# Optimization experiments

Measured on AMD Instinct MI355X. Metric: run time of the kernel, lower is better.

Reference implementation:

```python
import jax, jax.numpy as jnp
import numpy as np

N_NODES = 30000
N_EDGES = 480000
T_STEPS = 8
F_IN = 8
HID = 32
K = 5
PERIODS = 8


def setup_inputs() -> dict:
    key = jax.random.key(0)
    ks = jax.random.split(key, 9)
    timesteps = jax.random.normal(ks[0], (T_STEPS, N_NODES, F_IN), jnp.float32)
    src = jax.random.randint(ks[1], (N_EDGES,), 0, N_NODES)
    dst = jax.random.randint(ks[2], (N_EDGES,), 0, N_NODES)
    edge_index = jnp.stack([src, dst])
    # ChebConv weights for gates [i, f, c, o]; glorot-ish scale
    Wx = jax.random.normal(ks[3], (4, K, F_IN, HID), jnp.float32) * (1.0 / np.sqrt(F_IN))
    Wh = jax.random.normal(ks[4], (4, K, HID, HID), jnp.float32) * (1.0 / np.sqrt(HID))
    w_c = jax.random.normal(ks[5], (3, HID), jnp.float32) * 0.1  # peepholes for i, f, o
    b_gates = jax.random.normal(ks[6], (4, HID), jnp.float32) * 0.1  # b_i, b_f, b_c, b_o
    W_lin = jax.random.normal(ks[7], (PERIODS, HID), jnp.float32) * (1.0 / np.sqrt(HID))
    b_lin = jax.random.normal(ks[8], (PERIODS,), jnp.float32) * 0.1
    return {"timesteps": timesteps, "edge_index": edge_index, "Wx": Wx, "Wh": Wh,
            "w_c": w_c, "b_gates": b_gates, "W_lin": W_lin, "b_lin": b_lin}


def reference(timesteps, edge_index, Wx, Wh, w_c, b_gates, W_lin, b_lin):
    N = timesteps.shape[1]
    src, dst = edge_index[0], edge_index[1]
    # get_laplacian('sym') removes self loops, deg over edge rows; with lambda_max=2,
    # L_hat = 2L/lmax - I = -D^{-1/2} A D^{-1/2} (diag: 1 from L plus added -1 self loop = 0)
    w = jnp.where(src != dst, 1.0, 0.0).astype(timesteps.dtype)
    deg = jax.ops.segment_sum(w, src, num_segments=N)
    dis = jnp.where(deg > 0, 1.0 / jnp.sqrt(jnp.where(deg > 0, deg, 1.0)), 0.0)
    norm = dis[src] * w * dis[dst]  # [E]

    def lap(x):  # x: [N, C] -> L_hat @ x
        return -jax.ops.segment_sum(norm[:, None] * x[src], dst, num_segments=N)

    def cheb(x, W):  # Chebyshev recurrence; W: [K, in, out]
        Tx0 = x
        out = Tx0 @ W[0]
        Tx1 = lap(Tx0)
        out = out + Tx1 @ W[1]
        for k in range(2, W.shape[0]):
            Tx2 = 2.0 * lap(Tx1) - Tx0
            out = out + Tx2 @ W[k]
            Tx0, Tx1 = Tx1, Tx2
        return out

    def step(carry, x):
        H, C = carry
        I = jax.nn.sigmoid(cheb(x, Wx[0]) + cheb(H, Wh[0]) + w_c[0] * C + b_gates[0])
        Fg = jax.nn.sigmoid(cheb(x, Wx[1]) + cheb(H, Wh[1]) + w_c[1] * C + b_gates[1])
        Tg = jnp.tanh(cheb(x, Wx[2]) + cheb(H, Wh[2]) + b_gates[2])
        Cn = Fg * C + I * Tg
        O = jax.nn.sigmoid(cheb(x, Wx[3]) + cheb(H, Wh[3]) + w_c[2] * Cn + b_gates[3])
        Hn = O * jnp.tanh(Cn)
        return (Hn, Cn), None

    hid = Wh.shape[-1]
    H0 = jnp.zeros((N, hid), timesteps.dtype)
    (H, C), _ = jax.lax.scan(step, (H0, H0), timesteps)
    return jax.nn.relu(H) @ W_lin.T + b_lin
```

## Files before the change

### kernel.cpp

```cpp
#include <hip/hip_runtime.h>
#include <hip/hip_fp16.h>
#include <math.h>

#define T_STEPS 8
#define F_IN    8
#define HID     32
#define KCH     5
#define PERIODS 8

typedef __attribute__((ext_vector_type(8))) _Float16 half8_t;
typedef __attribute__((ext_vector_type(4))) float    f32x4_t;

__device__ __forceinline__ float sigmoidf_(float x) { return 1.f / (1.f + __expf(-x)); }
__device__ __forceinline__ float tanhf_(float x) {
    float e = __expf(2.f * x);
    return 1.f - 2.f / (e + 1.f);
}


__global__ void k_count(const int* __restrict__ src, const int* __restrict__ dst,
                        int* __restrict__ degi, int* __restrict__ cnt, int E) {
    int e = blockIdx.x * blockDim.x + threadIdx.x;
    if (e >= E) return;
    int s = src[e], d = dst[e];
    if (s != d) {
        atomicAdd(&degi[s], 1);
        atomicAdd(&cnt[d], 1);
    }
}

__global__ void k_hist2(const int* __restrict__ cnt, int* __restrict__ hist,
                        int N, int NT) {
    __shared__ int h[256];
    int tid = threadIdx.x, blk = blockIdx.x;
    h[tid] = 0;
    __syncthreads();
    int n = blk * 256 + tid;
    if (n < N) atomicAdd(&h[min(cnt[n], 255)], 1);
    __syncthreads();
    hist[tid * NT + blk] = h[tid];
}

__global__ void __launch_bounds__(1024) k_scan(const int* __restrict__ in,
                                               int* __restrict__ outp, int n) {
    __shared__ int wsum[16];
    int tid = threadIdx.x;
    int base = tid * 32;
    int v[32];
    int s = 0;
    #pragma unroll
    for (int i = 0; i < 32; ++i) {
        int idx = base + i;
        int t = (idx < n) ? in[idx] : 0;
        v[i] = t; s += t;
    }
    int lane = tid & 63, wave = tid >> 6;
    int incl = s;
    #pragma unroll
    for (int off = 1; off < 64; off <<= 1) {
        int t = __shfl_up(incl, off, 64);
        if (lane >= off) incl += t;
    }
    if (lane == 63) wsum[wave] = incl;
    __syncthreads();
    if (tid < 64) {
        int w = (tid < 16) ? wsum[tid] : 0;
        int iw = w;
        #pragma unroll
        for (int off = 1; off < 16; off <<= 1) {
            int t = __shfl_up(iw, off, 64);
            if (tid >= off) iw += t;
        }
        if (tid < 16) wsum[tid] = iw - w;
    }
    __syncthreads();
    int excl = wsum[wave] + (incl - s);
    #pragma unroll
    for (int i = 0; i < 32; ++i) {
        int idx = base + i;
        if (idx < n) outp[idx] = excl;
        excl += v[i];
    }
    if (tid == 1023) outp[n] = wsum[15] + incl;
}

__global__ void k_permscat2(const int* __restrict__ cnt, const int* __restrict__ degi,
                            const int* __restrict__ histbase,
                            int* __restrict__ perm, int* __restrict__ iperm,
                            int* __restrict__ cntp, float* __restrict__ dis,
                            int N, int NT) {
    __shared__ int key[256];
    int tid = threadIdx.x, blk = blockIdx.x;
    int n = blk * 256 + tid;
    int k = (n < N) ? min(cnt[n], 255) : -1;
    key[tid] = k;
    __syncthreads();
    if (n < N) {
        int r = 0;
        for (int j = 0; j < tid; ++j) r += (key[j] == k);
        int pos = histbase[k * NT + blk] + r;
        perm[pos] = n;
        iperm[n] = pos;
        cntp[pos] = cnt[n];
        int dg = degi[n];
        dis[n] = (dg > 0) ? rsqrtf((float)dg) : 0.f;
    }
}

__global__ void k_scatxt(const int* __restrict__ src, const int* __restrict__ dst,
                         const float* __restrict__ dis, const int* __restrict__ rowptr,
                         const int* __restrict__ iperm, int* __restrict__ fill,
                         unsigned int* __restrict__ cv, const float* __restrict__ xall,
                         __half* __restrict__ xb,
                         const float* __restrict__ Wh, __half* __restrict__ Bpack,
                         const float* __restrict__ Wx, __half* __restrict__ Bxpack,
                         int N, int E) {
    int gsz = (int)(gridDim.x * blockDim.x);
    int gtid = blockIdx.x * blockDim.x + threadIdx.x;
    for (int e = gtid; e < E; e += gsz) {
        int s = src[e], d = dst[e];
        if (s != d) {
            float nv = -dis[s] * dis[d];
            unsigned short h16 = __half_as_ushort(__float2half(nv));
            int dp = iperm[d];
            int p = atomicAdd(&fill[dp], 1);
            cv[rowptr[dp] + p] = (unsigned int)(unsigned short)iperm[s]
                               | ((unsigned int)h16 << 16);
        }
    }
    for (int i = gtid; i < N * T_STEPS; i += gsz) {
        int n = i >> 3, t = i & 7;
        float4 a = *(const float4*)(xall + ((size_t)t * N + n) * 8);
        float4 b = *(const float4*)(xall + ((size_t)t * N + n) * 8 + 4);
        __half2 h[4];
        h[0] = __float22half2_rn(make_float2(a.x, a.y));
        h[1] = __float22half2_rn(make_float2(a.z, a.w));
        h[2] = __float22half2_rn(make_float2(b.x, b.y));
        h[3] = __float22half2_rn(make_float2(b.z, b.w));
        *(float4*)(xb + (size_t)iperm[n] * 64 + t * 8) = *(float4*)h;
    }
    for (int i = gtid; i < KCH * 8 * 64 * 8; i += gsz) {
        int j = i & 7, lane = (i >> 3) & 63, nt = (i >> 9) & 7, k = i >> 12;
        int col = lane & 15, quad = lane >> 4;
        int kk = quad * 8 + j;
        int o = nt * 16 + col, g = o >> 5, h = o & 31;
        Bpack[i] = __float2half(Wh[(((g * KCH + k) * 32) + kk) * 32 + h]);
    }
    for (int i = gtid; i < 2 * 8 * 64 * 8; i += gsz) {
        int j = i & 7, lane = (i >> 3) & 63, nt = (i >> 9) & 7, c = i >> 12;
        int col = lane & 15, quad = lane >> 4;
        int kk = c * 32 + quad * 8 + j;
        int kcheb = kk >> 3, ch = kk & 7;
        int o = nt * 16 + col, g = o >> 5, h = o & 31;
        float v = (kcheb < KCH) ? Wx[(((g * KCH + kcheb) * 8) + ch) * 32 + h] : 0.f;
        Bxpack[i] = __float2half(v);
    }
}

template <int C, int ES>
__device__ __forceinline__ void lap_body(__half* __restrict__ outp,
                                         const __half* __restrict__ xin,
                                         const __half* __restrict__ xprev,
                                         float alpha, float beta,
                                         const int* __restrict__ rowptr,
                                         const unsigned int* __restrict__ cv,
                                         int N, int g) {
    constexpr int Q = C / 8;
    constexpr int W = Q * ES;
    int idx = g * 256 + (int)threadIdx.x;
    int node = idx / W;
    int r = idx % W;
    int q = r % Q, s = r / Q;
    if (node >= N) node = N - 1;
    int beg = rowptr[node], end = rowptr[node + 1];
    float a0 = 0.f, a1 = 0.f, a2 = 0.f, a3 = 0.f, a4 = 0.f, a5 = 0.f, a6 = 0.f, a7 = 0.f;
    #pragma unroll 8
    for (int j = beg + s; j < end; j += ES) {
        unsigned int pv = cv[j];
        int pcol = (int)(pv & 0xffffu);
        float nv = __half2float(__ushort_as_half((unsigned short)(pv >> 16)));
        float4 raw = *(const float4*)(xin + (size_t)pcol * C + q * 8);
        const __half2* h = (const __half2*)&raw;
        float2 f0 = __half22float2(h[0]);
        float2 f1 = __half22float2(h[1]);
        float2 f2 = __half22float2(h[2]);
        float2 f3 = __half22float2(h[3]);
        a0 += nv * f0.x; a1 += nv * f0.y; a2 += nv * f1.x; a3 += nv * f1.y;
        a4 += nv * f2.x; a5 += nv * f2.y; a6 += nv * f3.x; a7 += nv * f3.y;
    }
    #pragma unroll
    for (int m = Q; m < W; m <<= 1) {
        a0 += __shfl_xor(a0, m, 64); a1 += __shfl_xor(a1, m, 64);
        a2 += __shfl_xor(a2, m, 64); a3 += __shfl_xor(a3, m, 64);
        a4 += __shfl_xor(a4, m, 64); a5 += __shfl_xor(a5, m, 64);
        a6 += __shfl_xor(a6, m, 64); a7 += __shfl_xor(a7, m, 64);
    }
    if (s == 0) {
        size_t off = (size_t)node * C + q * 8;
        float r0 = alpha * a0, r1 = alpha * a1, r2 = alpha * a2, r3 = alpha * a3;
        float r4 = alpha * a4, r5 = alpha * a5, r6 = alpha * a6, r7 = alpha * a7;
        if (beta != 0.f) {
            float4 raw = *(const float4*)(xprev + off);
            const __half2* h = (const __half2*)&raw;
            float2 f0 = __half22float2(h[0]);
            float2 f1 = __half22float2(h[1]);
            float2 f2 = __half22float2(h[2]);
            float2 f3 = __half22float2(h[3]);
            r0 += beta * f0.x; r1 += beta * f0.y; r2 += beta * f1.x; r3 += beta * f1.y;
            r4 += beta * f2.x; r5 += beta * f2.y; r6 += beta * f3.x; r7 += beta * f3.y;
        }
        __half2 o[4];
        o[0] = __float22half2_rn(make_float2(r0, r1));
        o[1] = __float22half2_rn(make_float2(r2, r3));
        o[2] = __float22half2_rn(make_float2(r4, r5));
        o[3] = __float22half2_rn(make_float2(r6, r7));
        *(float4*)(outp + off) = *(float4*)o;
    }
}

template <int C, int ES>
__global__ void __launch_bounds__(256) k_lap_h(__half* __restrict__ outp,
                                               const __half* __restrict__ xin,
                                               const __half* __restrict__ xprev,
                                               float alpha, float beta,
                                               const int* __restrict__ rowptr,
                                               const unsigned int* __restrict__ cv,
                                               int N) {
    lap_body<C, ES>(outp, xin, xprev, alpha, beta, rowptr, cv, N, blockIdx.x);
}

__device__ __forceinline__ void step_body(
    const __half* __restrict__ xb, const __half* __restrict__ TXB,
    __half* __restrict__ THall, float* __restrict__ Cst,
    const __half* __restrict__ Bpack, const __half* __restrict__ Bxpack,
    const float* __restrict__ w_c, const float* __restrict__ bg,
    const float* __restrict__ W_lin, const float* __restrict__ b_lin,
    const int* __restrict__ perm, float* __restrict__ out,
    const int* __restrict__ rowptr, const unsigned int* __restrict__ cv,
    int t, int doOut, int N, int g,
    __half* __restrict__ T4s, float* __restrict__ FOs, float* __restrict__ Hs) {
    int tid = (int)threadIdx.x;
    int base = g * 16;
    int lane = tid & 63, wv = tid >> 6;
    int col = lane & 15, quad = lane >> 4;

    {
        const __half* T3 = THall + (size_t)3 * N * HID;
        const __half* T2 = THall + (size_t)2 * N * HID;
        int nl = tid >> 4;
        int r = tid & 15;
        int q = r & 3, s = r >> 2;
        int node = base + nl; if (node >= N) node = N - 1;
        int beg = rowptr[node], end = rowptr[node + 1];
        float a0 = 0.f, a1 = 0.f, a2 = 0.f, a3 = 0.f, a4 = 0.f, a5 = 0.f, a6 = 0.f, a7 = 0.f;
        #pragma unroll 8
        for (int j = beg + s; j < end; j += 4) {
            unsigned int pv = cv[j];
            int pcol = (int)(pv & 0xffffu);
            float nv = __half2float(__ushort_as_half((unsigned short)(pv >> 16)));
            float4 raw = *(const float4*)(T3 + (size_t)pcol * HID + q * 8);
            const __half2* h = (const __half2*)&raw;
            float2 f0 = __half22float2(h[0]);
            float2 f1 = __half22float2(h[1]);
            float2 f2 = __half22float2(h[2]);
            float2 f3 = __half22float2(h[3]);
            a0 += nv * f0.x; a1 += nv * f0.y; a2 += nv * f1.x; a3 += nv * f1.y;
            a4 += nv * f2.x; a5 += nv * f2.y; a6 += nv * f3.x; a7 += nv * f3.y;
        }
        #pragma unroll
        for (int m = 4; m < 16; m <<= 1) {
            a0 += __shfl_xor(a0, m, 64); a1 += __shfl_xor(a1, m, 64);
            a2 += __shfl_xor(a2, m, 64); a3 += __shfl_xor(a3, m, 64);
            a4 += __shfl_xor(a4, m, 64); a5 += __shfl_xor(a5, m, 64);
            a6 += __shfl_xor(a6, m, 64); a7 += __shfl_xor(a7, m, 64);
        }
        if (s == 0) {
            float4 raw = *(const float4*)(T2 + (size_t)node * HID + q * 8);
            const __half2* h = (const __half2*)&raw;
            float2 f0 = __half22float2(h[0]);
            float2 f1 = __half22float2(h[1]);
            float2 f2 = __half22float2(h[2]);
            float2 f3 = __half22float2(h[3]);
            __half2 o[4];
            o[0] = __float22half2_rn(make_float2(2.f * a0 - f0.x, 2.f * a1 - f0.y));
            o[1] = __float22half2_rn(make_float2(2.f * a2 - f1.x, 2.f * a3 - f1.y));
            o[2] = __float22half2_rn(make_float2(2.f * a4 - f2.x, 2.f * a5 - f2.y));
            o[3] = __float22half2_rn(make_float2(2.f * a6 - f3.x, 2.f * a7 - f3.y));
            *(float4*)(T4s + nl * 32 + q * 8) = *(float4*)o;
        }
    }
    __syncthreads();

    int node_a = base + col; if (node_a >= N) node_a = N - 1;
    f32x4_t acc[2];
    #pragma unroll
    for (int i = 0; i < 2; ++i) {
        float b = bg[(wv + 4 * i) * 16 + col];
        acc[i][0] = b; acc[i][1] = b; acc[i][2] = b; acc[i][3] = b;
    }
    const half8_t* Bx = (const half8_t*)Bxpack;
    const half8_t* Bp = (const half8_t*)Bpack;
    {
        const __half* sp0 = (quad == 0)
            ? (xb + (size_t)node_a * 64 + t * 8)
            : (TXB + ((size_t)(quad - 1) * N + node_a) * 64 + t * 8);
        half8_t ax0 = *(const half8_t*)sp0;
        half8_t ax1 = {};
        if (quad == 0)
            ax1 = *(const half8_t*)(TXB + ((size_t)3 * N + node_a) * 64 + t * 8);
        #pragma unroll
        for (int i = 0; i < 2; ++i) {
            int nt = wv + 4 * i;
            acc[i] = __builtin_amdgcn_mfma_f32_16x16x32_f16(ax0, Bx[nt * 64 + lane], acc[i], 0, 0, 0);
            acc[i] = __builtin_amdgcn_mfma_f32_16x16x32_f16(ax1, Bx[(8 + nt) * 64 + lane], acc[i], 0, 0, 0);
        }
    }
    #pragma unroll
    for (int k = 0; k < 4; ++k) {
        half8_t a = *(const half8_t*)(THall + ((size_t)k * N + node_a) * 32 + quad * 8);
        #pragma unroll
        for (int i = 0; i < 2; ++i) {
            int nt = wv + 4 * i;
            acc[i] = __builtin_amdgcn_mfma_f32_16x16x32_f16(a, Bp[(k * 8 + nt) * 64 + lane], acc[i], 0, 0, 0);
        }
    }
    {
        half8_t a = *(const half8_t*)(T4s + col * 32 + quad * 8);
        #pragma unroll
        for (int i = 0; i < 2; ++i) {
            int nt = wv + 4 * i;
            acc[i] = __builtin_amdgcn_mfma_f32_16x16x32_f16(a, Bp[(4 * 8 + nt) * 64 + lane], acc[i], 0, 0, 0);
        }
    }

    if (wv >= 2) {
        int h = (wv - 2) * 16 + col;
        #pragma unroll
        for (int reg = 0; reg < 4; ++reg) {
            int nl = quad * 4 + reg;
            FOs[nl * 64 + h]      = acc[0][reg];
            FOs[nl * 64 + 32 + h] = acc[1][reg];
        }
    }
    __syncthreads();

    if (wv < 2) {
        int h = wv * 16 + col;
        #pragma unroll
        for (int reg = 0; reg < 4; ++reg) {
            int nl = quad * 4 + reg;
            int node = base + nl;
            if (node < N) {
                size_t idx = (size_t)node * 32 + h;
                float Co = Cst[idx];
                float I  = sigmoidf_(acc[0][reg] + w_c[h] * Co);
                float F  = sigmoidf_(FOs[nl * 64 + h] + w_c[32 + h] * Co);
                float Tg = tanhf_(acc[1][reg]);
                float Cn = F * Co + I * Tg;
                float O  = sigmoidf_(FOs[nl * 64 + 32 + h] + w_c[64 + h] * Cn);
                float Hn = O * tanhf_(Cn);
                Cst[idx] = Cn;
                THall[idx] = __float2half(Hn);
                if (doOut) Hs[nl * 33 + h] = fmaxf(Hn, 0.f);
            } else if (doOut) {
                Hs[nl * 33 + h] = 0.f;
            }
        }
    }

    if (doOut) {
        __syncthreads();
        if (tid < 128) {
            int nl = tid >> 3, pp = tid & 7;
            int node = base + nl;
            if (node < N) {
                float a0 = b_lin[pp];
                const float* hp = Hs + nl * 33;
                #pragma unroll
                for (int h = 0; h < HID; ++h)
                    a0 += hp[h] * W_lin[pp * HID + h];
                out[(size_t)perm[node] * PERIODS + pp] = a0;
            }
        }
    }
}

__global__ void __launch_bounds__(256) k_lapstep(
    const __half* __restrict__ xb, const __half* __restrict__ TXB,
    __half* __restrict__ THall, float* __restrict__ Cst,
    const __half* __restrict__ Bpack, const __half* __restrict__ Bxpack,
    const float* __restrict__ w_c, const float* __restrict__ bg,
    const float* __restrict__ W_lin, const float* __restrict__ b_lin,
    const int* __restrict__ perm, float* __restrict__ out,
    const int* __restrict__ rowptr, const unsigned int* __restrict__ cv,
    int t, int doOut, int N) {
    __shared__ __half T4s[16 * 32];
    __shared__ float FOs[16 * 64];
    __shared__ float Hs[16 * 33];
    step_body(xb, TXB, THall, Cst, Bpack, Bxpack, w_c, bg, W_lin, b_lin,
              perm, out, rowptr, cv, t, doOut, N, blockIdx.x, T4s, FOs, Hs);
}

__device__ __forceinline__ void step0_body(
    const __half* __restrict__ xb, const __half* __restrict__ TXB,
    __half* __restrict__ TXB3, __half* __restrict__ THall, float* __restrict__ Cst,
    const __half* __restrict__ Bxpack,
    const float* __restrict__ w_c, const float* __restrict__ bg,
    const int* __restrict__ rowptr, const unsigned int* __restrict__ cv,
    int N, int g, __half* __restrict__ X3s, float* __restrict__ FOs) {
    int tid = (int)threadIdx.x;
    int base = g * 16;
    int lane = tid & 63, wv = tid >> 6;
    int col = lane & 15, quad = lane >> 4;

    {
        const __half* T2 = TXB + (size_t)2 * N * 64;
        const __half* T1 = TXB + (size_t)1 * N * 64;
        int nl = tid >> 4;
        int r = tid & 15;
        int q = r & 7, s = r >> 3;
        int node = base + nl; if (node >= N) node = N - 1;
        int beg = rowptr[node], end = rowptr[node + 1];
        float a0 = 0.f, a1 = 0.f, a2 = 0.f, a3 = 0.f, a4 = 0.f, a5 = 0.f, a6 = 0.f, a7 = 0.f;
        #pragma unroll 8
        for (int j = beg + s; j < end; j += 2) {
            unsigned int pv = cv[j];
            int pcol = (int)(pv & 0xffffu);
            float nv = __half2float(__ushort_as_half((unsigned short)(pv >> 16)));
            float4 raw = *(const float4*)(T2 + (size_t)pcol * 64 + q * 8);
            const __half2* h = (const __half2*)&raw;
            float2 f0 = __half22float2(h[0]);
            float2 f1 = __half22float2(h[1]);
            float2 f2 = __half22float2(h[2]);
            float2 f3 = __half22float2(h[3]);
            a0 += nv * f0.x; a1 += nv * f0.y; a2 += nv * f1.x; a3 += nv * f1.y;
            a4 += nv * f2.x; a5 += nv * f2.y; a6 += nv * f3.x; a7 += nv * f3.y;
        }
        a0 += __shfl_xor(a0, 8, 64); a1 += __shfl_xor(a1, 8, 64);
        a2 += __shfl_xor(a2, 8, 64); a3 += __shfl_xor(a3, 8, 64);
        a4 += __shfl_xor(a4, 8, 64); a5 += __shfl_xor(a5, 8, 64);
        a6 += __shfl_xor(a6, 8, 64); a7 += __shfl_xor(a7, 8, 64);
        if (s == 0) {
            size_t off = (size_t)node * 64 + q * 8;
            float4 raw = *(const float4*)(T1 + off);
            const __half2* h = (const __half2*)&raw;
            float2 f0 = __half22float2(h[0]);
            float2 f1 = __half22float2(h[1]);
            float2 f2 = __half22float2(h[2]);
            float2 f3 = __half22float2(h[3]);
            __half2 o[4];
            o[0] = __float22half2_rn(make_float2(2.f * a0 - f0.x, 2.f * a1 - f0.y));
            o[1] = __float22half2_rn(make_float2(2.f * a2 - f1.x, 2.f * a3 - f1.y));
            o[2] = __float22half2_rn(make_float2(2.f * a4 - f2.x, 2.f * a5 - f2.y));
            o[3] = __float22half2_rn(make_float2(2.f * a6 - f3.x, 2.f * a7 - f3.y));
            *(float4*)(TXB3 + off) = *(float4*)o;
            *(float4*)(X3s + nl * 64 + q * 8) = *(float4*)o;
        }
    }
    __syncthreads();

    int node_a = base + col; if (node_a >= N) node_a = N - 1;
    f32x4_t acc[2];
    #pragma unroll
    for (int i = 0; i < 2; ++i) {
        float b = bg[(wv + 4 * i) * 16 + col];
        acc[i][0] = b; acc[i][1] = b; acc[i][2] = b; acc[i][3] = b;
    }
    const half8_t* Bx = (const half8_t*)Bxpack;
    {
        const __half* sp0 = (quad == 0)
            ? (xb + (size_t)node_a * 64)
            : (TXB + ((size_t)(quad - 1) * N + node_a) * 64);
        half8_t ax0 = *(const half8_t*)sp0;
        half8_t ax1 = {};
        if (quad == 0)
            ax1 = *(const half8_t*)(X3s + col * 64);
        #pragma unroll
        for (int i = 0; i < 2; ++i) {
            int nt = wv + 4 * i;
            acc[i] = __builtin_amdgcn_mfma_f32_16x16x32_f16(ax0, Bx[nt * 64 + lane], acc[i], 0, 0, 0);
            acc[i] = __builtin_amdgcn_mfma_f32_16x16x32_f16(ax1, Bx[(8 + nt) * 64 + lane], acc[i], 0, 0, 0);
        }
    }
    __syncthreads();

    if (wv >= 2) {
        int h = (wv - 2) * 16 + col;
        #pragma unroll
        for (int reg = 0; reg < 4; ++reg) {
            int nl = quad * 4 + reg;
            FOs[nl * 64 + h]      = acc[0][reg];
            FOs[nl * 64 + 32 + h] = acc[1][reg];
        }
    }
    __syncthreads();

    if (wv < 2) {
        int h = wv * 16 + col;
        #pragma unroll
        for (int reg = 0; reg < 4; ++reg) {
            int nl = quad * 4 + reg;
            int node = base + nl;
            if (node < N) {
                size_t idx = (size_t)node * 32 + h;
                float I  = sigmoidf_(acc[0][reg]);
                float Tg = tanhf_(acc[1][reg]);
                float Cn = I * Tg;
                float O  = sigmoidf_(FOs[nl * 64 + 32 + h] + w_c[64 + h] * Cn);
                Cst[idx] = Cn;
                THall[idx] = __float2half(O * tanhf_(Cn));
            }
        }
    }
}

__global__ void __launch_bounds__(256) k_lapstep0(
    const __half* __restrict__ xb, const __half* __restrict__ TXB,
    __half* __restrict__ TXB3, __half* __restrict__ THall, float* __restrict__ Cst,
    const __half* __restrict__ Bxpack,
    const float* __restrict__ w_c, const float* __restrict__ bg,
    const int* __restrict__ rowptr, const unsigned int* __restrict__ cv, int N) {
    __shared__ float FOs[16 * 64];
    step0_body(xb, TXB, TXB3, THall, Cst, Bxpack, w_c, bg, rowptr, cv, N,
               blockIdx.x, (__half*)FOs, FOs);
}


extern "C" void kernel_launch(void* const* d_in, const int* in_sizes, int n_in,
                              void* d_out, int out_size, void* d_ws, size_t ws_size,
                              hipStream_t stream) {
    const float* xall  = (const float*)d_in[0];
    const int*   ei    = (const int*)d_in[1];
    const float* Wx    = (const float*)d_in[2];
    const float* Wh    = (const float*)d_in[3];
    const float* w_c   = (const float*)d_in[4];
    const float* bg    = (const float*)d_in[5];
    const float* W_lin = (const float*)d_in[6];
    const float* b_lin = (const float*)d_in[7];
    float* out = (float*)d_out;

    const int E = in_sizes[1] / 2;
    const int N = in_sizes[0] / (T_STEPS * F_IN);
    const int NT = (N + 255) / 256;
    const int* src = ei;
    const int* dst = ei + E;

    char* p = (char*)d_ws;
    auto carve = [&](size_t bytes) -> void* {
        void* r = (void*)p;
        p += (bytes + 255) & ~(size_t)255;
        return r;
    };
    char* zero_begin = p;
    int*    degi  = (int*)   carve((size_t)N * 4);
    int*    cnt   = (int*)   carve((size_t)N * 4);
    int*    fill  = (int*)   carve((size_t)N * 4);
    float*  Cst   = (float*) carve((size_t)N * HID * 4);
    size_t zero_bytes = (size_t)(p - zero_begin);
    __half* THall = (__half*)carve((size_t)4 * N * HID * 2);
    int*    hist     = (int*)   carve((size_t)256 * NT * 4);
    int*    histbase = (int*)   carve(((size_t)256 * NT + 1) * 4);
    float*  dis      = (float*) carve((size_t)N * 4);
    int*    perm     = (int*)   carve((size_t)N * 4);
    int*    iperm    = (int*)   carve((size_t)N * 4);
    int*    cntp     = (int*)   carve((size_t)N * 4);
    int*    rowptr   = (int*)   carve((size_t)(N + 1) * 4);
    unsigned int* cv = (unsigned int*)carve((size_t)E * 4);
    __half* xb       = (__half*)carve((size_t)N * 64 * 2);
    __half* TXB      = (__half*)carve((size_t)4 * N * 64 * 2);
    __half* Bpack    = (__half*)carve((size_t)KCH * 8 * 64 * 8 * 2);
    __half* Bxpack   = (__half*)carve((size_t)2 * 8 * 64 * 8 * 2);

    hipMemsetAsync(zero_begin, 0, zero_bytes, stream);

    const int TB = 256;
    const int gE = (E + TB - 1) / TB;
    k_count<<<gE, TB, 0, stream>>>(src, dst, degi, cnt, E);
    k_hist2<<<NT, TB, 0, stream>>>(cnt, hist, N, NT);
    k_scan<<<1, 1024, 0, stream>>>(hist, histbase, 256 * NT);
    k_permscat2<<<NT, TB, 0, stream>>>(cnt, degi, histbase, perm, iperm, cntp, dis, N, NT);
    k_scan<<<1, 1024, 0, stream>>>(cntp, rowptr, N);
    k_scatxt<<<gE, TB, 0, stream>>>(src, dst, dis, rowptr, iperm, fill, cv, xall, xb,
                                    Wh, Bpack, Wx, Bxpack, N, E);

    __half* TXB0 = TXB;
    __half* TXB1 = TXB + (size_t)N * 64;
    __half* TXB2 = TXB + (size_t)2 * N * 64;
    __half* TXB3 = TXB + (size_t)3 * N * 64;
    const int lapx_grid = (N * 8 + TB - 1) / TB;
    k_lap_h<64, 1><<<lapx_grid, TB, 0, stream>>>(TXB0, xb,   nullptr, 1.f,  0.f, rowptr, cv, N);
    k_lap_h<64, 1><<<lapx_grid, TB, 0, stream>>>(TXB1, TXB0, xb,      2.f, -1.f, rowptr, cv, N);
    k_lap_h<64, 1><<<lapx_grid, TB, 0, stream>>>(TXB2, TXB1, TXB0,    2.f, -1.f, rowptr, cv, N);

    const int lapstep_grid = (N + 15) / 16;
    const int laph_grid = (N * 8 + TB - 1) / TB;
    __half* TH0 = THall;
    __half* TH1 = THall + (size_t)N * HID;
    __half* TH2 = THall + (size_t)2 * N * HID;
    __half* TH3 = THall + (size_t)3 * N * HID;

    k_lapstep0<<<lapstep_grid, TB, 0, stream>>>(xb, TXB, TXB3, THall, Cst, Bxpack,
                                                w_c, bg, rowptr, cv, N);
    for (int t = 1; t < T_STEPS; ++t) {
        k_lap_h<HID, 2><<<laph_grid, TB, 0, stream>>>(TH1, TH0, nullptr, 1.f,  0.f, rowptr, cv, N);
        k_lap_h<HID, 2><<<laph_grid, TB, 0, stream>>>(TH2, TH1, TH0,     2.f, -1.f, rowptr, cv, N);
        k_lap_h<HID, 2><<<laph_grid, TB, 0, stream>>>(TH3, TH2, TH1,     2.f, -1.f, rowptr, cv, N);
        k_lapstep<<<lapstep_grid, TB, 0, stream>>>(xb, TXB, THall, Cst, Bpack, Bxpack,
                                                   w_c, bg, W_lin, b_lin, perm, out,
                                                   rowptr, cv, t,
                                                   (t == T_STEPS - 1) ? 1 : 0, N);
    }
}
```

Baseline: 588.1 us.

## Drop degree-sorted node permutation and shrink step kernels to 128 threads

Removes the histogram, bucket sort and permutation kernels that reordered nodes by in-degree. CSR is now built directly in original node order with fewer preprocessing launches, and the dis computation moves into the scan kernel. The fused step kernels drop from 256 to 128 threads, with each wave holding all four gate accumulators, so the shared-memory exchange of the F/O gates and one barrier go away. The cost is losing degree-sorted load balance and locality in the gather kernels, and each step block now has less parallelism per node.

```diff
diff --git a/kernel.cpp b/kernel.cpp
--- a/kernel.cpp
+++ b/kernel.cpp
@@ -18,114 +18,19 @@
 }
 
 
-__global__ void k_count(const int* __restrict__ src, const int* __restrict__ dst,
-                        int* __restrict__ degi, int* __restrict__ cnt, int E) {
-    int e = blockIdx.x * blockDim.x + threadIdx.x;
-    if (e >= E) return;
-    int s = src[e], d = dst[e];
-    if (s != d) {
-        atomicAdd(&degi[s], 1);
-        atomicAdd(&cnt[d], 1);
-    }
-}
-
-__global__ void k_hist2(const int* __restrict__ cnt, int* __restrict__ hist,
-                        int N, int NT) {
-    __shared__ int h[256];
-    int tid = threadIdx.x, blk = blockIdx.x;
-    h[tid] = 0;
-    __syncthreads();
-    int n = blk * 256 + tid;
-    if (n < N) atomicAdd(&h[min(cnt[n], 255)], 1);
-    __syncthreads();
-    hist[tid * NT + blk] = h[tid];
-}
-
-__global__ void __launch_bounds__(1024) k_scan(const int* __restrict__ in,
-                                               int* __restrict__ outp, int n) {
-    __shared__ int wsum[16];
-    int tid = threadIdx.x;
-    int base = tid * 32;
-    int v[32];
-    int s = 0;
-    #pragma unroll
-    for (int i = 0; i < 32; ++i) {
-        int idx = base + i;
-        int t = (idx < n) ? in[idx] : 0;
-        v[i] = t; s += t;
-    }
-    int lane = tid & 63, wave = tid >> 6;
-    int incl = s;
-    #pragma unroll
-    for (int off = 1; off < 64; off <<= 1) {
-        int t = __shfl_up(incl, off, 64);
-        if (lane >= off) incl += t;
-    }
-    if (lane == 63) wsum[wave] = incl;
-    __syncthreads();
-    if (tid < 64) {
-        int w = (tid < 16) ? wsum[tid] : 0;
-        int iw = w;
-        #pragma unroll
-        for (int off = 1; off < 16; off <<= 1) {
-            int t = __shfl_up(iw, off, 64);
-            if (tid >= off) iw += t;
-        }
-        if (tid < 16) wsum[tid] = iw - w;
-    }
-    __syncthreads();
-    int excl = wsum[wave] + (incl - s);
-    #pragma unroll
-    for (int i = 0; i < 32; ++i) {
-        int idx = base + i;
-        if (idx < n) outp[idx] = excl;
-        excl += v[i];
-    }
-    if (tid == 1023) outp[n] = wsum[15] + incl;
-}
-
-__global__ void k_permscat2(const int* __restrict__ cnt, const int* __restrict__ degi,
-                            const int* __restrict__ histbase,
-                            int* __restrict__ perm, int* __restrict__ iperm,
-                            int* __restrict__ cntp, float* __restrict__ dis,
-                            int N, int NT) {
-    __shared__ int key[256];
-    int tid = threadIdx.x, blk = blockIdx.x;
-    int n = blk * 256 + tid;
-    int k = (n < N) ? min(cnt[n], 255) : -1;
-    key[tid] = k;
-    __syncthreads();
-    if (n < N) {
-        int r = 0;
-        for (int j = 0; j < tid; ++j) r += (key[j] == k);
-        int pos = histbase[k * NT + blk] + r;
-        perm[pos] = n;
-        iperm[n] = pos;
-        cntp[pos] = cnt[n];
-        int dg = degi[n];
-        dis[n] = (dg > 0) ? rsqrtf((float)dg) : 0.f;
-    }
-}
-
-__global__ void k_scatxt(const int* __restrict__ src, const int* __restrict__ dst,
-                         const float* __restrict__ dis, const int* __restrict__ rowptr,
-                         const int* __restrict__ iperm, int* __restrict__ fill,
-                         unsigned int* __restrict__ cv, const float* __restrict__ xall,
-                         __half* __restrict__ xb,
-                         const float* __restrict__ Wh, __half* __restrict__ Bpack,
-                         const float* __restrict__ Wx, __half* __restrict__ Bxpack,
-                         int N, int E) {
+__global__ void k_prep(const int* __restrict__ src, const int* __restrict__ dst,
+                       int* __restrict__ degi, int* __restrict__ cnt,
+                       const float* __restrict__ xall, __half* __restrict__ xb,
+                       const float* __restrict__ Wh, __half* __restrict__ Bpack,
+                       const float* __restrict__ Wx, __half* __restrict__ Bxpack,
+                       int N, int E) {
     int gsz = (int)(gridDim.x * blockDim.x);
     int gtid = blockIdx.x * blockDim.x + threadIdx.x;
     for (int e = gtid; e < E; e += gsz) {
         int s = src[e], d = dst[e];
         if (s != d) {
-            float nv = -dis[s] * dis[d];
-            unsigned short h16 = __half_as_ushort(__float2half(nv));
-            int dp = iperm[d];
-            int p = atomicAdd(&fill[dp], 1);
-            cv[rowptr[dp] + p] = (unsigned int)(unsigned short)iperm[s]
-                               | ((unsigned int)h16 << 16);
+            atomicAdd(&degi[s], 1);
+            atomicAdd(&cnt[d], 1);
         }
     }
     for (int i = gtid; i < N * T_STEPS; i += gsz) {
@@ -137,7 +42,7 @@
         h[1] = __float22half2_rn(make_float2(a.z, a.w));
         h[2] = __float22half2_rn(make_float2(b.x, b.y));
         h[3] = __float22half2_rn(make_float2(b.z, b.w));
-        *(float4*)(xb + (size_t)iperm[n] * 64 + t * 8) = *(float4*)h;
+        *(float4*)(xb + (size_t)n * 64 + t * 8) = *(float4*)h;
     }
     for (int i = gtid; i < KCH * 8 * 64 * 8; i += gsz) {
         int j = i & 7, lane = (i >> 3) & 63, nt = (i >> 9) & 7, k = i >> 12;
@@ -154,6 +59,72 @@
         int o = nt * 16 + col, g = o >> 5, h = o & 31;
         float v = (kcheb < KCH) ? Wx[(((g * KCH + kcheb) * 8) + ch) * 32 + h] : 0.f;
         Bxpack[i] = __float2half(v);
+    }
+}
+
+__global__ void __launch_bounds__(1024) k_scan2(const int* __restrict__ in,
+                                                int* __restrict__ outp, int n,
+                                                const int* __restrict__ degi,
+                                                float* __restrict__ dis) {
+    __shared__ int wsum[16];
+    int tid = threadIdx.x;
+    for (int i = tid; i < n; i += 1024) {
+        int dg = degi[i];
+        dis[i] = (dg > 0) ? rsqrtf((float)dg) : 0.f;
+    }
+    int base = tid * 32;
+    int v[32];
+    int s = 0;
+    #pragma unroll
+    for (int i = 0; i < 32; ++i) {
+        int idx = base + i;
+        int t = (idx < n) ? in[idx] : 0;
+        v[i] = t; s += t;
+    }
+    int lane = tid & 63, wave = tid >> 6;
+    int incl = s;
+    #pragma unroll
+    for (int off = 1; off < 64; off <<= 1) {
+        int t = __shfl_up(incl, off, 64);
+        if (lane >= off) incl += t;
+    }
+    if (lane == 63) wsum[wave] = incl;
+    __syncthreads();
+    if (tid < 64) {
+        int w = (tid < 16) ? wsum[tid] : 0;
+        int iw = w;
+        #pragma unroll
+        for (int off = 1; off < 16; off <<= 1) {
+            int t = __shfl_up(iw, off, 64);
+            if (tid >= off) iw += t;
+        }
+        if (tid < 16) wsum[tid] = iw - w;
+    }
+    __syncthreads();
+    int excl = wsum[wave] + (incl - s);
+    #pragma unroll
+    for (int i = 0; i < 32; ++i) {
+        int idx = base + i;
+        if (idx < n) outp[idx] = excl;
+        excl += v[i];
+    }
+    if (tid == 1023) outp[n] = wsum[15] + incl;
+}
+
+__global__ void k_scat(const int* __restrict__ src, const int* __restrict__ dst,
+                       const float* __restrict__ dis, const int* __restrict__ rowptr,
+                       int* __restrict__ fill, unsigned int* __restrict__ cv, int E) {
+    int gsz = (int)(gridDim.x * blockDim.x);
+    int gtid = blockIdx.x * blockDim.x + threadIdx.x;
+    for (int e = gtid; e < E; e += gsz) {
+        int s = src[e], d = dst[e];
+        if (s != d) {
+            float nv = -dis[s] * dis[d];
+            unsigned short h16 = __half_as_ushort(__float2half(nv));
+            int p = atomicAdd(&fill[d], 1);
+            cv[rowptr[d] + p] = (unsigned int)(unsigned short)s
+                              | ((unsigned int)h16 << 16);
+        }
     }
 }
 
@@ -235,26 +206,26 @@
     const __half* __restrict__ Bpack, const __half* __restrict__ Bxpack,
     const float* __restrict__ w_c, const float* __restrict__ bg,
     const float* __restrict__ W_lin, const float* __restrict__ b_lin,
-    const int* __restrict__ perm, float* __restrict__ out,
+    float* __restrict__ out,
     const int* __restrict__ rowptr, const unsigned int* __restrict__ cv,
     int t, int doOut, int N, int g,
-    __half* __restrict__ T4s, float* __restrict__ FOs, float* __restrict__ Hs) {
+    __half* __restrict__ T4s, float* __restrict__ Hs) {
     int tid = (int)threadIdx.x;
     int base = g * 16;
-    int lane = tid & 63, wv = tid >> 6;
+    int lane = tid & 63, w = tid >> 6;
     int col = lane & 15, quad = lane >> 4;
 
     {
         const __half* T3 = THall + (size_t)3 * N * HID;
         const __half* T2 = THall + (size_t)2 * N * HID;
-        int nl = tid >> 4;
-        int r = tid & 15;
+        int nl = tid >> 3;
+        int r = tid & 7;
         int q = r & 3, s = r >> 2;
         int node = base + nl; if (node >= N) node = N - 1;
         int beg = rowptr[node], end = rowptr[node + 1];
         float a0 = 0.f, a1 = 0.f, a2 = 0.f, a3 = 0.f, a4 = 0.f, a5 = 0.f, a6 = 0.f, a7 = 0.f;
         #pragma unroll 8
-        for (int j = beg + s; j < end; j += 4) {
+        for (int j = beg + s; j < end; j += 2) {
             unsigned int pv = cv[j];
             int pcol = (int)(pv & 0xffffu);
             float nv = __half2float(__ushort_as_half((unsigned short)(pv >> 16)));
@@ -267,13 +238,10 @@
             a0 += nv * f0.x; a1 += nv * f0.y; a2 += nv * f1.x; a3 += nv * f1.y;
             a4 += nv * f2.x; a5 += nv * f2.y; a6 += nv * f3.x; a7 += nv * f3.y;
         }
-        #pragma unroll
-        for (int m = 4; m < 16; m <<= 1) {
-            a0 += __shfl_xor(a0, m, 64); a1 += __shfl_xor(a1, m, 64);
-            a2 += __shfl_xor(a2, m, 64); a3 += __shfl_xor(a3, m, 64);
-            a4 += __shfl_xor(a4, m, 64); a5 += __shfl_xor(a5, m, 64);
-            a6 += __shfl_xor(a6, m, 64); a7 += __shfl_xor(a7, m, 64);
-        }
+        a0 += __shfl_xor(a0, 4, 64); a1 += __shfl_xor(a1, 4, 64);
+        a2 += __shfl_xor(a2, 4, 64); a3 += __shfl_xor(a3, 4, 64);
+        a4 += __shfl_xor(a4, 4, 64); a5 += __shfl_xor(a5, 4, 64);
+        a6 += __shfl_xor(a6, 4, 64); a7 += __shfl_xor(a7, 4, 64);
         if (s == 0) {
             float4 raw = *(const float4*)(T2 + (size_t)node * HID + q * 8);
             const __half2* h = (const __half2*)&raw;
@@ -292,11 +260,11 @@
     __syncthreads();
 
     int node_a = base + col; if (node_a >= N) node_a = N - 1;
-    f32x4_t acc[2];
-    #pragma unroll
-    for (int i = 0; i < 2; ++i) {
-        float b = bg[(wv + 4 * i) * 16 + col];
-        acc[i][0] = b; acc[i][1] = b; acc[i][2] = b; acc[i][3] = b;
+    f32x4_t acc[4];
+    #pragma unroll
+    for (int gi = 0; gi < 4; ++gi) {
+        float b = bg[(2 * gi + w) * 16 + col];
+        acc[gi][0] = b; acc[gi][1] = b; acc[gi][2] = b; acc[gi][3] = b;
     }
     const half8_t* Bx = (const half8_t*)Bxpack;
     const half8_t* Bp = (const half8_t*)Bpack;
@@ -309,43 +277,32 @@
         if (quad == 0)
             ax1 = *(const half8_t*)(TXB + ((size_t)3 * N + node_a) * 64 + t * 8);
         #pragma unroll
-        for (int i = 0; i < 2; ++i) {
-            int nt = wv + 4 * i;
-            acc[i] = __builtin_amdgcn_mfma_f32_16x16x32_f16(ax0, Bx[nt * 64 + lane], acc[i], 0, 0, 0);
-            acc[i] = __builtin_amdgcn_mfma_f32_16x16x32_f16(ax1, Bx[(8 + nt) * 64 + lane], acc[i], 0, 0, 0);
+        for (int gi = 0; gi < 4; ++gi) {
+            int nt = 2 * gi + w;
+            acc[gi] = __builtin_amdgcn_mfma_f32_16x16x32_f16(ax0, Bx[nt * 64 + lane], acc[gi], 0, 0, 0);
+            acc[gi] = __builtin_amdgcn_mfma_f32_16x16x32_f16(ax1, Bx[(8 + nt) * 64 + lane], acc[gi], 0, 0, 0);
         }
     }
     #pragma unroll
     for (int k = 0; k < 4; ++k) {
         half8_t a = *(const half8_t*)(THall + ((size_t)k * N + node_a) * 32 + quad * 8);
         #pragma unroll
-        for (int i = 0; i < 2; ++i) {
-            int nt = wv + 4 * i;
-            acc[i] = __builtin_amdgcn_mfma_f32_16x16x32_f16(a, Bp[(k * 8 + nt) * 64 + lane], acc[i], 0, 0, 0);
+        for (int gi = 0; gi < 4; ++gi) {
+            int nt = 2 * gi + w;
+            acc[gi] = __builtin_amdgcn_mfma_f32_16x16x32_f16(a, Bp[(k * 8 + nt) * 64 + lane], acc[gi], 0, 0, 0);
         }
     }
     {
         half8_t a = *(const half8_t*)(T4s + col * 32 + quad * 8);
         #pragma unroll
-        for (int i = 0; i < 2; ++i) {
-            int nt = wv + 4 * i;
-            acc[i] = __builtin_amdgcn_mfma_f32_16x16x32_f16(a, Bp[(4 * 8 + nt) * 64 + lane], acc[i], 0, 0, 0);
-        }
-    }
-
-    if (wv >= 2) {
-        int h = (wv - 2) * 16 + col;
-        #pragma unroll
-        for (int reg = 0; reg < 4; ++reg) {
-            int nl = quad * 4 + reg;
-            FOs[nl * 64 + h]      = acc[0][reg];
-            FOs[nl * 64 + 32 + h] = acc[1][reg];
-        }
-    }
-    __syncthreads();
-
-    if (wv < 2) {
-        int h = wv * 16 + col;
+        for (int gi = 0; gi < 4; ++gi) {
+            int nt = 2 * gi + w;
+            acc[gi] = __builtin_amdgcn_mfma_f32_16x16x32_f16(a, Bp[(4 * 8 + nt) * 64 + lane], acc[gi], 0, 0, 0);
+        }
+    }
+
+    {
+        int h = w * 16 + col;
         #pragma unroll
         for (int reg = 0; reg < 4; ++reg) {
             int nl = quad * 4 + reg;
@@ -354,10 +311,10 @@
                 size_t idx = (size_t)node * 32 + h;
                 float Co = Cst[idx];
                 float I  = sigmoidf_(acc[0][reg] + w_c[h] * Co);
-                float F  = sigmoidf_(FOs[nl * 64 + h] + w_c[32 + h] * Co);
-                float Tg = tanhf_(acc[1][reg]);
+                float F  = sigmoidf_(acc[1][reg] + w_c[32 + h] * Co);
+                float Tg = tanhf_(acc[2][reg]);
                 float Cn = F * Co + I * Tg;
-                float O  = sigmoidf_(FOs[nl * 64 + 32 + h] + w_c[64 + h] * Cn);
+                float O  = sigmoidf_(acc[3][reg] + w_c[64 + h] * Cn);
                 float Hn = O * tanhf_(Cn);
                 Cst[idx] = Cn;
                 THall[idx] = __float2half(Hn);
@@ -370,35 +327,32 @@
 
     if (doOut) {
         __syncthreads();
-        if (tid < 128) {
-            int nl = tid >> 3, pp = tid & 7;
-            int node = base + nl;
-            if (node < N) {
-                float a0 = b_lin[pp];
-                const float* hp = Hs + nl * 33;
-                #pragma unroll
-                for (int h = 0; h < HID; ++h)
-                    a0 += hp[h] * W_lin[pp * HID + h];
-                out[(size_t)perm[node] * PERIODS + pp] = a0;
-            }
-        }
-    }
-}
-
-__global__ void __launch_bounds__(256) k_lapstep(
+        int nl = tid >> 3, pp = tid & 7;
+        int node = base + nl;
+        if (node < N) {
+            float a0 = b_lin[pp];
+            const float* hp = Hs + nl * 33;
+            #pragma unroll
+            for (int h = 0; h < HID; ++h)
+                a0 += hp[h] * W_lin[pp * HID + h];
+            out[(size_t)node * PERIODS + pp] = a0;
+        }
+    }
+}
+
+__global__ void __launch_bounds__(128) k_lapstep(
     const __half* __restrict__ xb, const __half* __restrict__ TXB,
     __half* __restrict__ THall, float* __restrict__ Cst,
     const __half* __restrict__ Bpack, const __half* __restrict__ Bxpack,
     const float* __restrict__ w_c, const float* __restrict__ bg,
     const float* __restrict__ W_lin, const float* __restrict__ b_lin,
-    const int* __restrict__ perm, float* __restrict__ out,
+    float* __restrict__ out,
     const int* __restrict__ rowptr, const unsigned int* __restrict__ cv,
     int t, int doOut, int N) {
     __shared__ __half T4s[16 * 32];
-    __shared__ float FOs[16 * 64];
     __shared__ float Hs[16 * 33];
     step_body(xb, TXB, THall, Cst, Bpack, Bxpack, w_c, bg, W_lin, b_lin,
-              perm, out, rowptr, cv, t, doOut, N, blockIdx.x, T4s, FOs, Hs);
+              out, rowptr, cv, t, doOut, N, blockIdx.x, T4s, Hs);
 }
 
 __device__ __forceinline__ void step0_body(
@@ -407,23 +361,22 @@
     const __half* __restrict__ Bxpack,
     const float* __restrict__ w_c, const float* __restrict__ bg,
     const int* __restrict__ rowptr, const unsigned int* __restrict__ cv,
-    int N, int g, __half* __restrict__ X3s, float* __restrict__ FOs) {
+    int N, int g, __half* __restrict__ X3s) {
     int tid = (int)threadIdx.x;
     int base = g * 16;
-    int lane = tid & 63, wv = tid >> 6;
+    int lane = tid & 63, w = tid >> 6;
     int col = lane & 15, quad = lane >> 4;
 
     {
         const __half* T2 = TXB + (size_t)2 * N * 64;
         const __half* T1 = TXB + (size_t)1 * N * 64;
-        int nl = tid >> 4;
-        int r = tid & 15;
-        int q = r & 7, s = r >> 3;
+        int nl = tid >> 3;
+        int q = tid & 7;
         int node = base + nl; if (node >= N) node = N - 1;
         int beg = rowptr[node], end = rowptr[node + 1];
         float a0 = 0.f, a1 = 0.f, a2 = 0.f, a3 = 0.f, a4 = 0.f, a5 = 0.f, a6 = 0.f, a7 = 0.f;
         #pragma unroll 8
-        for (int j = beg + s; j < end; j += 2) {
+        for (int j = beg; j < end; ++j) {
             unsigned int pv = cv[j];
             int pcol = (int)(pv & 0xffffu);
             float nv = __half2float(__ushort_as_half((unsigned short)(pv >> 16)));
@@ -436,35 +389,29 @@
             a0 += nv * f0.x; a1 += nv * f0.y; a2 += nv * f1.x; a3 += nv * f1.y;
             a4 += nv * f2.x; a5 += nv * f2.y; a6 += nv * f3.x; a7 += nv * f3.y;
         }
-        a0 += __shfl_xor(a0, 8, 64); a1 += __shfl_xor(a1, 8, 64);
-        a2 += __shfl_xor(a2, 8, 64); a3 += __shfl_xor(a3, 8, 64);
-        a4 += __shfl_xor(a4, 8, 64); a5 += __shfl_xor(a5, 8, 64);
-        a6 += __shfl_xor(a6, 8, 64); a7 += __shfl_xor(a7, 8, 64);
-        if (s == 0) {
-            size_t off = (size_t)node * 64 + q * 8;
-            float4 raw = *(const float4*)(T1 + off);
-            const __half2* h = (const __half2*)&raw;
-            float2 f0 = __half22float2(h[0]);
-            float2 f1 = __half22float2(h[1]);
-            float2 f2 = __half22float2(h[2]);
-            float2 f3 = __half22float2(h[3]);
-            __half2 o[4];
-            o[0] = __float22half2_rn(make_float2(2.f * a0 - f0.x, 2.f * a1 - f0.y));
-            o[1] = __float22half2_rn(make_float2(2.f * a2 - f1.x, 2.f * a3 - f1.y));
-            o[2] = __float22half2_rn(make_float2(2.f * a4 - f2.x, 2.f * a5 - f2.y));
-            o[3] = __float22half2_rn(make_float2(2.f * a6 - f3.x, 2.f * a7 - f3.y));
-            *(float4*)(TXB3 + off) = *(float4*)o;
-            *(float4*)(X3s + nl * 64 + q * 8) = *(float4*)o;
-        }
+        size_t off = (size_t)node * 64 + q * 8;
+        float4 raw = *(const float4*)(T1 + off);
+        const __half2* h = (const __half2*)&raw;
+        float2 f0 = __half22float2(h[0]);
+        float2 f1 = __half22float2(h[1]);
+        float2 f2 = __half22float2(h[2]);
+        float2 f3 = __half22float2(h[3]);
+        __half2 o[4];
+        o[0] = __float22half2_rn(make_float2(2.f * a0 - f0.x, 2.f * a1 - f0.y));
+        o[1] = __float22half2_rn(make_float2(2.f * a2 - f1.x, 2.f * a3 - f1.y));
+        o[2] = __float22half2_rn(make_float2(2.f * a4 - f2.x, 2.f * a5 - f2.y));
+        o[3] = __float22half2_rn(make_float2(2.f * a6 - f3.x, 2.f * a7 - f3.y));
+        *(float4*)(TXB3 + off) = *(float4*)o;
+        *(float4*)(X3s + nl * 64 + q * 8) = *(float4*)o;
     }
     __syncthreads();
 
     int node_a = base + col; if (node_a >= N) node_a = N - 1;
-    f32x4_t acc[2];
-    #pragma unroll
-    for (int i = 0; i < 2; ++i) {
-        float b = bg[(wv + 4 * i) * 16 + col];
-        acc[i][0] = b; acc[i][1] = b; acc[i][2] = b; acc[i][3] = b;
+    f32x4_t acc[4];
+    #pragma unroll
+    for (int gi = 0; gi < 4; ++gi) {
+        float b = bg[(2 * gi + w) * 16 + col];
+        acc[gi][0] = b; acc[gi][1] = b; acc[gi][2] = b; acc[gi][3] = b;
     }
     const half8_t* Bx = (const half8_t*)Bxpack;
     {
@@ -476,27 +423,15 @@
         if (quad == 0)
             ax1 = *(const half8_t*)(X3s + col * 64);
         #pragma unroll
-        for (int i = 0; i < 2; ++i) {
-            int nt = wv + 4 * i;
-            acc[i] = __builtin_amdgcn_mfma_f32_16x16x32_f16(ax0, Bx[nt * 64 + lane], acc[i], 0, 0, 0);
-            acc[i] = __builtin_amdgcn_mfma_f32_16x16x32_f16(ax1, Bx[(8 + nt) * 64 + lane], acc[i], 0, 0, 0);
-        }
-    }
-    __syncthreads();
-
-    if (wv >= 2) {
-        int h = (wv - 2) * 16 + col;
-        #pragma unroll
-        for (int reg = 0; reg < 4; ++reg) {
-            int nl = quad * 4 + reg;
-            FOs[nl * 64 + h]      = acc[0][reg];
-            FOs[nl * 64 + 32 + h] = acc[1][reg];
-        }
-    }
-    __syncthreads();
-
-    if (wv < 2) {
-        int h = wv * 16 + col;
+        for (int gi = 0; gi < 4; ++gi) {
+            int nt = 2 * gi + w;
+            acc[gi] = __builtin_amdgcn_mfma_f32_16x16x32_f16(ax0, Bx[nt * 64 + lane], acc[gi], 0, 0, 0);
+            acc[gi] = __builtin_amdgcn_mfma_f32_16x16x32_f16(ax1, Bx[(8 + nt) * 64 + lane], acc[gi], 0, 0, 0);
+        }
+    }
+
+    {
+        int h = w * 16 + col;
         #pragma unroll
         for (int reg = 0; reg < 4; ++reg) {
             int nl = quad * 4 + reg;
@@ -504,9 +439,9 @@
             if (node < N) {
                 size_t idx = (size_t)node * 32 + h;
                 float I  = sigmoidf_(acc[0][reg]);
-                float Tg = tanhf_(acc[1][reg]);
+                float Tg = tanhf_(acc[2][reg]);
                 float Cn = I * Tg;
-                float O  = sigmoidf_(FOs[nl * 64 + 32 + h] + w_c[64 + h] * Cn);
+                float O  = sigmoidf_(acc[3][reg] + w_c[64 + h] * Cn);
                 Cst[idx] = Cn;
                 THall[idx] = __float2half(O * tanhf_(Cn));
             }
@@ -514,15 +449,15 @@
     }
 }
 
-__global__ void __launch_bounds__(256) k_lapstep0(
+__global__ void __launch_bounds__(128) k_lapstep0(
     const __half* __restrict__ xb, const __half* __restrict__ TXB,
     __half* __restrict__ TXB3, __half* __restrict__ THall, float* __restrict__ Cst,
     const __half* __restrict__ Bxpack,
     const float* __restrict__ w_c, const float* __restrict__ bg,
     const int* __restrict__ rowptr, const unsigned int* __restrict__ cv, int N) {
-    __shared__ float FOs[16 * 64];
+    __shared__ __half X3s[16 * 64];
     step0_body(xb, TXB, TXB3, THall, Cst, Bxpack, w_c, bg, rowptr, cv, N,
-               blockIdx.x, (__half*)FOs, FOs);
+               blockIdx.x, X3s);
 }
 
 
@@ -541,7 +476,6 @@
 
     const int E = in_sizes[1] / 2;
     const int N = in_sizes[0] / (T_STEPS * F_IN);
-    const int NT = (N + 255) / 256;
     const int* src = ei;
     const int* dst = ei + E;
 
@@ -558,12 +492,7 @@
     float*  Cst   = (float*) carve((size_t)N * HID * 4);
     size_t zero_bytes = (size_t)(p - zero_begin);
     __half* THall = (__half*)carve((size_t)4 * N * HID * 2);
-    int*    hist     = (int*)   carve((size_t)256 * NT * 4);
-    int*    histbase = (int*)   carve(((size_t)256 * NT + 1) * 4);
     float*  dis      = (float*) carve((size_t)N * 4);
-    int*    perm     = (int*)   carve((size_t)N * 4);
-    int*    iperm    = (int*)   carve((size_t)N * 4);
-    int*    cntp     = (int*)   carve((size_t)N * 4);
     int*    rowptr   = (int*)   carve((size_t)(N + 1) * 4);
     unsigned int* cv = (unsigned int*)carve((size_t)E * 4);
     __half* xb       = (__half*)carve((size_t)N * 64 * 2);
@@ -575,13 +504,10 @@
 
     const int TB = 256;
     const int gE = (E + TB - 1) / TB;
-    k_count<<<gE, TB, 0, stream>>>(src, dst, degi, cnt, E);
-    k_hist2<<<NT, TB, 0, stream>>>(cnt, hist, N, NT);
-    k_scan<<<1, 1024, 0, stream>>>(hist, histbase, 256 * NT);
-    k_permscat2<<<NT, TB, 0, stream>>>(cnt, degi, histbase, perm, iperm, cntp, dis, N, NT);
-    k_scan<<<1, 1024, 0, stream>>>(cntp, rowptr, N);
-    k_scatxt<<<gE, TB, 0, stream>>>(src, dst, dis, rowptr, iperm, fill, cv, xall, xb,
-                                    Wh, Bpack, Wx, Bxpack, N, E);
+    k_prep<<<gE, TB, 0, stream>>>(src, dst, degi, cnt, xall, xb,
+                                  Wh, Bpack, Wx, Bxpack, N, E);
+    k_scan2<<<1, 1024, 0, stream>>>(cnt, rowptr, N, degi, dis);
+    k_scat<<<gE, TB, 0, stream>>>(src, dst, dis, rowptr, fill, cv, E);
 
     __half* TXB0 = TXB;
     __half* TXB1 = TXB + (size_t)N * 64;
@@ -599,15 +525,15 @@
     __half* TH2 = THall + (size_t)2 * N * HID;
     __half* TH3 = THall + (size_t)3 * N * HID;
 
-    k_lapstep0<<<lapstep_grid, TB, 0, stream>>>(xb, TXB, TXB3, THall, Cst, Bxpack,
-                                                w_c, bg, rowptr, cv, N);
+    k_lapstep0<<<lapstep_grid, 128, 0, stream>>>(xb, TXB, TXB3, THall, Cst, Bxpack,
+                                                 w_c, bg, rowptr, cv, N);
     for (int t = 1; t < T_STEPS; ++t) {
         k_lap_h<HID, 2><<<laph_grid, TB, 0, stream>>>(TH1, TH0, nullptr, 1.f,  0.f, rowptr, cv, N);
         k_lap_h<HID, 2><<<laph_grid, TB, 0, stream>>>(TH2, TH1, TH0,     2.f, -1.f, rowptr, cv, N);
         k_lap_h<HID, 2><<<laph_grid, TB, 0, stream>>>(TH3, TH2, TH1,     2.f, -1.f, rowptr, cv, N);
-        k_lapstep<<<lapstep_grid, TB, 0, stream>>>(xb, TXB, THall, Cst, Bpack, Bxpack,
-                                                   w_c, bg, W_lin, b_lin, perm, out,
-                                                   rowptr, cv, t,
-                                                   (t == T_STEPS - 1) ? 1 : 0, N);
-    }
-}
+        k_lapstep<<<lapstep_grid, 128, 0, stream>>>(xb, TXB, THall, Cst, Bpack, Bxpack,
+                                                    w_c, bg, W_lin, b_lin, out,
+                                                    rowptr, cv, t,
+                                                    (t == T_STEPS - 1) ? 1 : 0, N);
+    }
+}
```

After: 562.8 us. 1.04x faster.
